# Kernel optimization log

Hardware: AMD Instinct MI355X
Metric: run time of the kernel (lower is better)

The kernel has to match this reference:

```python
import jax, jax.numpy as jnp
import numpy as np

I = 100000      # item_count
U = 131072      # user_count
E = 64          # embeddings_size
K = 3           # convolution_depth
TOPK = 15       # top_k nonzeros per row of S
NNZ_S = I * TOPK
NNZ_U = 4194304 # user-item interactions
KEEP = 0.8      # 1 - user_profile_dropout


def setup_inputs() -> dict:
    key = jax.random.key(0)
    k1, k2, k3, k4, k5, k6 = jax.random.split(key, 6)
    return {
        "item_emb": jax.random.normal(k1, (I, E), dtype=jnp.float32),
        "S_vals": jax.random.uniform(k2, (NNZ_S,), dtype=jnp.float32),
        "S_rows": jnp.sort(jax.random.randint(k3, (NNZ_S,), 0, I, dtype=jnp.int32)),
        "S_cols": jax.random.randint(k4, (NNZ_S,), 0, I, dtype=jnp.int32),
        "urm_vals": jnp.ones((NNZ_U,), dtype=jnp.float32),
        "urm_rows": jnp.sort(jax.random.randint(k5, (NNZ_U,), 0, U, dtype=jnp.int32)),
        "urm_cols": jax.random.randint(k6, (NNZ_U,), 0, I, dtype=jnp.int32),
    }


def _spmm(vals, rows, cols, x, n_rows):
    # sparse (COO) @ dense: gather source rows, scale by edge value, scatter-add.
    return jax.ops.segment_sum(vals[:, None] * x[cols], rows, num_segments=n_rows)


def reference(item_emb, S_vals, urm_vals, S_rows, S_cols, urm_rows, urm_cols):
    # sparse dropout on URM values (tf_dropout_sparse: drop + rescale by 1/keep)
    mask = jax.random.bernoulli(jax.random.key(42), KEEP, urm_vals.shape)
    uv = jnp.where(mask, urm_vals / KEEP, 0.0)
    # k-hop item-graph convolution: x <- S @ x, repeated K times
    x = item_emb
    for _ in range(K):
        x = _spmm(S_vals, S_rows, S_cols, x, I)
    # user embeddings: URM @ x
    user_emb = _spmm(uv, urm_rows, urm_cols, x, U)
    return user_emb, x
```

## Files before the change

### kernel.cpp

```cpp
#include <hip/hip_runtime.h>
#include <hip/hip_fp16.h>

#define I_CNT 100000
#define U_CNT 131072
#define E_DIM 64
#define IE (I_CNT * E_DIM)
#define UE ((size_t)U_CNT * E_DIM)

#define DEPTH 32

__device__ __forceinline__ unsigned rotl32(unsigned v, int n) {
    return (v << n) | (v >> (32 - n));
}
__device__ __forceinline__ void threefry2x32(unsigned k0, unsigned k1,
                                             unsigned x0, unsigned x1,
                                             unsigned& o0, unsigned& o1) {
    unsigned k2 = k0 ^ k1 ^ 0x1BD11BDAu;
    x0 += k0; x1 += k1;
#define RND(r) { x0 += x1; x1 = rotl32(x1, r); x1 ^= x0; }
    RND(13) RND(15) RND(26) RND(6)   x0 += k1; x1 += k2 + 1u;
    RND(17) RND(29) RND(16) RND(24)  x0 += k2; x1 += k0 + 2u;
    RND(13) RND(15) RND(26) RND(6)   x0 += k0; x1 += k1 + 3u;
    RND(17) RND(29) RND(16) RND(24)  x0 += k1; x1 += k2 + 4u;
    RND(13) RND(15) RND(26) RND(6)   x0 += k2; x1 += k0 + 5u;
#undef RND
    o0 = x0; o1 = x1;
}

__device__ __forceinline__ float dropout_mul(unsigned e) {
    unsigned o0, o1;
    threefry2x32(0u, 42u, 0u, e, o0, o1);
    const unsigned bits = o0 ^ o1;
    const float u = __uint_as_float((bits >> 9) | 0x3f800000u) - 1.0f;
    return (u < 0.8f) ? 1.25f : 0.0f;
}

__device__ __forceinline__ int rl_i(int v, int l) {
    return __builtin_amdgcn_readlane(v, l);
}
__device__ __forceinline__ float rl_f(float v, int l) {
    return __int_as_float(__builtin_amdgcn_readlane(__float_as_int(v), l));
}

__device__ __forceinline__ float2 unpack_h2(unsigned u) {
    float2 f;
    f.x = __half2float(__ushort_as_half((unsigned short)(u & 0xffffu)));
    f.y = __half2float(__ushort_as_half((unsigned short)(u >> 16)));
    return f;
}
__device__ __forceinline__ unsigned pack_h2(float a, float b) {
    const unsigned ha = __half_as_ushort(__float2half(a));
    const unsigned hb = __half_as_ushort(__float2half(b));
    return ha | (hb << 16);
}

__global__ void build_row_ptr(const int* __restrict__ rows,
                              int* __restrict__ row_ptr,
                              int nnz, int n_rows) {
    const int e = blockIdx.x * blockDim.x + threadIdx.x;
    if (e >= nnz) return;
    const int r  = rows[e];
    const int rp = (e == 0) ? -1 : rows[e - 1];
    for (int q = rp + 1; q <= r; ++q) row_ptr[q] = e;
    if (e == nnz - 1) {
        for (int q = r + 1; q <= n_rows; ++q) row_ptr[q] = nnz;
    }
}

__global__ __launch_bounds__(256) void f32_to_f16_vec(const float4* __restrict__ in,
                                                      unsigned long long* __restrict__ out,
                                                      int n4) {
    const int i = blockIdx.x * blockDim.x + threadIdx.x;
    if (i >= n4) return;
    const float4 f = in[i];
    const unsigned long long lo = pack_h2(f.x, f.y);
    const unsigned long long hi = pack_h2(f.z, f.w);
    __builtin_nontemporal_store(lo | (hi << 32), &out[i]);
}

template <bool DROPOUT, int NROWS, int SLOTS, bool OUT32, bool OUT16>
__global__ __launch_bounds__(256) void spmm_q(const float* __restrict__ vals,
                                              const int* __restrict__ row_ptr,
                                              const int* __restrict__ cols,
                                              const unsigned short* __restrict__ xh,
                                              float* __restrict__ y32,
                                              unsigned short* __restrict__ y16,
                                              int n_rows, int nnz) {
    constexpr int T     = NROWS * SLOTS;
    constexpr int QUADS = T / 4;
    constexpr int QPR   = SLOTS / 4;
    static_assert(T <= 64 && (SLOTS % 4) == 0, "slots must quad-align");

    const int lane = threadIdx.x & 63;
    const int wave = blockIdx.x * (blockDim.x >> 6) + (threadIdx.x >> 6);
    const int r0   = wave * NROWS;
    if (r0 >= n_rows) return;

    const int q  = min(lane / SLOTS, NROWS - 1);
    const int jr = lane - q * SLOTS;
    const int rq = r0 + q;

    const int s   = row_ptr[rq];
    const int e   = row_ptr[rq + 1];
    const int len = e - s;

    int ce = s + min(jr, max(len - 1, 0));
    ce = min(ce, nnz - 1);
    const int idx = __builtin_nontemporal_load(&cols[ce]);
    float v;
    {
        const int ve = min(s + jr, nnz - 1);
        float vv = __builtin_nontemporal_load(&vals[ve]);
        if (DROPOUT) vv *= dropout_mul((unsigned)ve);
        v = (jr < len) ? vv : 0.0f;
    }
    const int coff = idx << 7;

    const int g    = lane >> 4;
    const int m    = lane & 15;
    const int moff = m << 3;
    const char* __restrict__ xb = (const char*)xh;

    float4 ovf[NROWS];
#pragma unroll
    for (int qq = 0; qq < NROWS; ++qq) ovf[qq] = make_float4(0.f, 0.f, 0.f, 0.f);
    if (__any(len > SLOTS)) {
#pragma unroll
        for (int qq = 0; qq < NROWS; ++qq) {
            const int rs = rl_i(s, qq * SLOTS);
            const int re = rl_i(e, qq * SLOTS);
            for (int t = rs + SLOTS; t < re; ++t) {
                if (g == 0) {
                    const int c = cols[t];
                    float vv = vals[t];
                    if (DROPOUT) vv *= dropout_mul((unsigned)t);
                    const uint2 u = *(const uint2*)(xb + (c << 7) + moff);
                    const float2 f01 = unpack_h2(u.x);
                    const float2 f23 = unpack_h2(u.y);
                    ovf[qq].x = fmaf(vv, f01.x, ovf[qq].x);
                    ovf[qq].y = fmaf(vv, f01.y, ovf[qq].y);
                    ovf[qq].z = fmaf(vv, f23.x, ovf[qq].z);
                    ovf[qq].w = fmaf(vv, f23.y, ovf[qq].w);
                }
            }
        }
    }

    uint2 xq[QUADS];
#pragma unroll
    for (int k = 0; k < QUADS; ++k) {
        const int co = __shfl(coff, 4 * k + g);
        xq[k] = *(const uint2*)(xb + co + moff);
    }

    float4 acc = make_float4(0.f, 0.f, 0.f, 0.f);
#pragma unroll
    for (int k = 0; k < QUADS; ++k) {
        const float vv = __shfl(v, 4 * k + g);
        const float2 f01 = unpack_h2(xq[k].x);
        const float2 f23 = unpack_h2(xq[k].y);
        acc.x = fmaf(vv, f01.x, acc.x);
        acc.y = fmaf(vv, f01.y, acc.y);
        acc.z = fmaf(vv, f23.x, acc.z);
        acc.w = fmaf(vv, f23.y, acc.w);
        if ((k % QPR) == QPR - 1) {
            const int qk = k / QPR;
            float ax = acc.x + ovf[qk].x;
            float ay = acc.y + ovf[qk].y;
            float az = acc.z + ovf[qk].z;
            float aw = acc.w + ovf[qk].w;
            ax += __shfl_xor(ax, 16); ax += __shfl_xor(ax, 32);
            ay += __shfl_xor(ay, 16); ay += __shfl_xor(ay, 32);
            az += __shfl_xor(az, 16); az += __shfl_xor(az, 32);
            aw += __shfl_xor(aw, 16); aw += __shfl_xor(aw, 32);
            const size_t rowoff = ((size_t)(r0 + qk)) << 6;
            if (lane < 16) {
                if constexpr (OUT32) {
                    *(float4*)(y32 + rowoff + (m << 2)) = make_float4(ax, ay, az, aw);
                }
            } else if (lane < 32) {
                if constexpr (OUT16) {
                    const unsigned px = pack_h2(ax, ay);
                    const unsigned py = pack_h2(az, aw);
                    *(uint2*)(y16 + rowoff + (m << 2)) = make_uint2(px, py);
                }
            }
            acc = make_float4(0.f, 0.f, 0.f, 0.f);
        }
    }
    (void)y32; (void)y16;
}

template <bool DROPOUT, int NROWS, int SLOTS>
__global__ __launch_bounds__(256) void spmm_slots(const float* __restrict__ vals,
                                                  const int* __restrict__ row_ptr,
                                                  const int* __restrict__ cols,
                                                  const float* __restrict__ x,
                                                  float* __restrict__ y,
                                                  int n_rows, int nnz) {
    constexpr int T = NROWS * SLOTS;
    static_assert(T <= 64, "slots must fit one wave");
    constexpr int RING = (DEPTH < T) ? DEPTH : T;

    const int lane = threadIdx.x & 63;
    const int wave = blockIdx.x * (blockDim.x >> 6) + (threadIdx.x >> 6);
    const int r0   = wave * NROWS;
    if (r0 >= n_rows) return;

    const int q  = min(lane / SLOTS, NROWS - 1);
    const int j  = lane - q * SLOTS;
    const int rq = r0 + q;

    const int s   = row_ptr[rq];
    const int e   = row_ptr[rq + 1];
    const int len = e - s;

    int ce = s + min(j, max(len - 1, 0));
    ce = min(ce, nnz - 1);
    const int idx = cols[ce];
    float v;
    {
        const int ve = min(s + j, nnz - 1);
        float vv = vals[ve];
        if (DROPOUT) vv *= dropout_mul((unsigned)ve);
        v = (j < len) ? vv : 0.0f;
    }

    float ovf[NROWS];
#pragma unroll
    for (int qq = 0; qq < NROWS; ++qq) ovf[qq] = 0.0f;
    if (__any(len > SLOTS)) {
#pragma unroll
        for (int qq = 0; qq < NROWS; ++qq) {
            const int rs = rl_i(s, qq * SLOTS);
            const int re = rl_i(e, qq * SLOTS);
            for (int t = rs + SLOTS; t < re; ++t) {
                const int c = cols[t];
                float vv = vals[t];
                if (DROPOUT) vv *= dropout_mul((unsigned)t);
                ovf[qq] = fmaf(vv, x[((size_t)(unsigned)c << 6) + lane], ovf[qq]);
            }
        }
    }

    float xv[RING];
#pragma unroll
    for (int u = 0; u < RING; ++u) {
        xv[u] = x[((size_t)(unsigned)rl_i(idx, u) << 6) + lane];
    }

    float acc = 0.0f;
#pragma unroll
    for (int k = 0; k < T; ++k) {
        const float xc = xv[k % RING];
        if (k + RING < T) {
            xv[k % RING] = x[((size_t)(unsigned)rl_i(idx, k + RING) << 6) + lane];
        }
        acc = fmaf(rl_f(v, k), xc, acc);
        if ((k % SLOTS) == SLOTS - 1) {
            const int qk = k / SLOTS;
            y[((size_t)(r0 + qk) << 6) + lane] = acc + ovf[qk];
            acc = 0.0f;
        }
    }
}

static inline int blocks_for_waves(int waves) {
    return (waves + 3) / 4;
}

extern "C" void kernel_launch(void* const* d_in, const int* in_sizes, int n_in,
                              void* d_out, int out_size, void* d_ws, size_t ws_size,
                              hipStream_t stream) {
    const float* item_emb = (const float*)d_in[0];
    const float* S_vals   = (const float*)d_in[1];
    const int*   S_rows   = (const int*)  d_in[2];
    const int*   S_cols   = (const int*)  d_in[3];
    const float* urm_vals = (const float*)d_in[4];
    const int*   urm_rows = (const int*)  d_in[5];
    const int*   urm_cols = (const int*)  d_in[6];

    const int nnzS = in_sizes[1];
    const int nnzU = in_sizes[4];

    float* user_out = (float*)d_out;
    float* x_out    = (float*)d_out + UE;

    const size_t rpS_bytes = ((size_t)(I_CNT + 1) * sizeof(int) + 255) & ~(size_t)255;
    const size_t rpU_bytes = ((size_t)(U_CNT + 1) * sizeof(int) + 255) & ~(size_t)255;
    const size_t h_bytes   = (size_t)IE * sizeof(unsigned short);
    int* rpS = (int*)d_ws;
    int* rpU = (int*)((char*)d_ws + rpS_bytes);
    unsigned short* hA = (unsigned short*)((char*)d_ws + rpS_bytes + rpU_bytes);
    unsigned short* hB = (unsigned short*)((char*)hA + h_bytes);
    const size_t need = rpS_bytes + rpU_bytes + 2 * h_bytes;

    const dim3 blk(256);

    build_row_ptr<<<(nnzS + 255) / 256, blk, 0, stream>>>(S_rows, rpS, nnzS, I_CNT);
    build_row_ptr<<<(nnzU + 255) / 256, blk, 0, stream>>>(urm_rows, rpU, nnzU, U_CNT);

    const int wS = I_CNT / 2;

    if (ws_size >= need) {
        f32_to_f16_vec<<<(IE / 4 + 255) / 256, blk, 0, stream>>>(
            (const float4*)item_emb, (unsigned long long*)hA, IE / 4);

        spmm_q<false, 2, 24, false, true><<<blocks_for_waves(wS), blk, 0, stream>>>(
            S_vals, rpS, S_cols, hA, nullptr, hB, I_CNT, nnzS);
        spmm_q<false, 2, 24, false, true><<<blocks_for_waves(wS), blk, 0, stream>>>(
            S_vals, rpS, S_cols, hB, nullptr, hA, I_CNT, nnzS);
        spmm_q<false, 2, 24, true, true><<<blocks_for_waves(wS), blk, 0, stream>>>(
            S_vals, rpS, S_cols, hA, x_out, hB, I_CNT, nnzS);
        spmm_q<true, 1, 48, true, false><<<blocks_for_waves(U_CNT), blk, 0, stream>>>(
            urm_vals, rpU, urm_cols, hB, user_out, nullptr, U_CNT, nnzU);
    } else {
        spmm_slots<false, 2, 24><<<blocks_for_waves(wS), blk, 0, stream>>>(
            S_vals, rpS, S_cols, item_emb, x_out, I_CNT, nnzS);
        spmm_slots<false, 2, 24><<<blocks_for_waves(wS), blk, 0, stream>>>(
            S_vals, rpS, S_cols, x_out, user_out, I_CNT, nnzS);
        spmm_slots<false, 2, 24><<<blocks_for_waves(wS), blk, 0, stream>>>(
            S_vals, rpS, S_cols, user_out, x_out, I_CNT, nnzS);
        spmm_slots<true, 1, 48><<<blocks_for_waves(U_CNT), blk, 0, stream>>>(
            urm_vals, rpU, urm_cols, x_out, user_out, U_CNT, nnzU);
    }
}
```

Measured before the change: 303.8 us.

## Split embedding columns into four phases with blocked fp16 layout for cache reuse

The fp16 embedding buffers are rearranged into four column blocks of 16 features, each stored contiguously per row. Every SpMM now launches four phase-separated grids, each gathering only a 32-byte slice per row, so the gathered working set of each phase is small enough to stay cache-resident. The cost is that row pointers, columns and values are re-read once per phase, and each gathered row segment is now a narrower 32-byte access. A separate pre-pass also applies the URM dropout mask once up front, so the user SpMM no longer evaluates the random generator inline.

Measured after the change: 580.6 us. +91.1%, slower.

```diff
diff --git a/kernel.cpp b/kernel.cpp
--- a/kernel.cpp
+++ b/kernel.cpp
@@ -7,6 +7,7 @@
 #define IE (I_CNT * E_DIM)
 #define UE ((size_t)U_CNT * E_DIM)
 
+#define NPH 4
 #define DEPTH 32
 
 __device__ __forceinline__ unsigned rotl32(unsigned v, int n) {
@@ -67,59 +68,73 @@
     }
 }
 
-__global__ __launch_bounds__(256) void f32_to_f16_vec(const float4* __restrict__ in,
-                                                      unsigned long long* __restrict__ out,
+__global__ __launch_bounds__(256) void mask_vals(const float* __restrict__ vals,
+                                                 float* __restrict__ out, int nnz) {
+    const int e = blockIdx.x * blockDim.x + threadIdx.x;
+    if (e >= nnz) return;
+    __builtin_nontemporal_store(vals[e] * dropout_mul((unsigned)e), &out[e]);
+}
+
+__global__ __launch_bounds__(256) void f32_to_f16_blk(const float4* __restrict__ in,
+                                                      unsigned short* __restrict__ out,
                                                       int n4) {
     const int i = blockIdx.x * blockDim.x + threadIdx.x;
     if (i >= n4) return;
+    const int r   = i >> 4;
+    const int ii  = i & 15;
+    const int blk = ii >> 2;
+    const int mm  = ii & 3;
     const float4 f = in[i];
     const unsigned long long lo = pack_h2(f.x, f.y);
     const unsigned long long hi = pack_h2(f.z, f.w);
-    __builtin_nontemporal_store(lo | (hi << 32), &out[i]);
+    unsigned short* dst = out + ((size_t)blk * I_CNT + r) * 16 + (mm << 2);
+    __builtin_nontemporal_store(lo | (hi << 32), (unsigned long long*)dst);
 }
 
 template <bool DROPOUT, int NROWS, int SLOTS, bool OUT32, bool OUT16>
-__global__ __launch_bounds__(256) void spmm_q(const float* __restrict__ vals,
-                                              const int* __restrict__ row_ptr,
-                                              const int* __restrict__ cols,
-                                              const unsigned short* __restrict__ xh,
-                                              float* __restrict__ y32,
-                                              unsigned short* __restrict__ y16,
-                                              int n_rows, int nnz) {
-    constexpr int T     = NROWS * SLOTS;
-    constexpr int QUADS = T / 4;
-    constexpr int QPR   = SLOTS / 4;
-    static_assert(T <= 64 && (SLOTS % 4) == 0, "slots must quad-align");
-
-    const int lane = threadIdx.x & 63;
-    const int wave = blockIdx.x * (blockDim.x >> 6) + (threadIdx.x >> 6);
-    const int r0   = wave * NROWS;
+__global__ __launch_bounds__(256) void spmm_ph(const float* __restrict__ vals,
+                                               const int* __restrict__ row_ptr,
+                                               const int* __restrict__ cols,
+                                               const unsigned short* __restrict__ xh,
+                                               float* __restrict__ y32,
+                                               unsigned short* __restrict__ y16,
+                                               int n_rows, int nnz, int bpp) {
+    constexpr int T   = NROWS * SLOTS;
+    constexpr int LDN = T / 16;
+    constexpr int LPR = SLOTS / 16;
+    static_assert(T <= 64 && (SLOTS % 16) == 0, "slots must 16-align");
+
+    const int lane  = threadIdx.x & 63;
+    const int phase = blockIdx.x / bpp;
+    const int lblk  = blockIdx.x - phase * bpp;
+    const int wave  = lblk * (blockDim.x >> 6) + (threadIdx.x >> 6);
+    const int r0    = wave * NROWS;
     if (r0 >= n_rows) return;
 
     const int q  = min(lane / SLOTS, NROWS - 1);
-    const int jr = lane - q * SLOTS;
+    const int j  = lane - q * SLOTS;
     const int rq = r0 + q;
 
     const int s   = row_ptr[rq];
     const int e   = row_ptr[rq + 1];
     const int len = e - s;
 
-    int ce = s + min(jr, max(len - 1, 0));
+    int ce = s + min(j, max(len - 1, 0));
     ce = min(ce, nnz - 1);
     const int idx = __builtin_nontemporal_load(&cols[ce]);
     float v;
     {
-        const int ve = min(s + jr, nnz - 1);
+        const int ve = min(s + j, nnz - 1);
         float vv = __builtin_nontemporal_load(&vals[ve]);
         if (DROPOUT) vv *= dropout_mul((unsigned)ve);
-        v = (jr < len) ? vv : 0.0f;
-    }
-    const int coff = idx << 7;
-
-    const int g    = lane >> 4;
-    const int m    = lane & 15;
-    const int moff = m << 3;
-    const char* __restrict__ xb = (const char*)xh;
+        v = (j < len) ? vv : 0.0f;
+    }
+    const int coff = idx << 5;
+
+    const int g = lane >> 2;
+    const int m = lane & 3;
+    const char* __restrict__ xb =
+        (const char*)xh + (size_t)phase * ((size_t)I_CNT * 32);
 
     float4 ovf[NROWS];
 #pragma unroll
@@ -134,7 +149,7 @@
                     const int c = cols[t];
                     float vv = vals[t];
                     if (DROPOUT) vv *= dropout_mul((unsigned)t);
-                    const uint2 u = *(const uint2*)(xb + (c << 7) + moff);
+                    const uint2 u = *(const uint2*)(xb + (c << 5) + (m << 3));
                     const float2 f01 = unpack_h2(u.x);
                     const float2 f23 = unpack_h2(u.y);
                     ovf[qq].x = fmaf(vv, f01.x, ovf[qq].x);
@@ -146,43 +161,48 @@
         }
     }
 
-    uint2 xq[QUADS];
-#pragma unroll
-    for (int k = 0; k < QUADS; ++k) {
-        const int co = __shfl(coff, 4 * k + g);
-        xq[k] = *(const uint2*)(xb + co + moff);
+    uint2 xq[LDN];
+#pragma unroll
+    for (int k = 0; k < LDN; ++k) {
+        const int co = __shfl(coff, 16 * k + g);
+        xq[k] = *(const uint2*)(xb + co + (m << 3));
     }
 
     float4 acc = make_float4(0.f, 0.f, 0.f, 0.f);
 #pragma unroll
-    for (int k = 0; k < QUADS; ++k) {
-        const float vv = __shfl(v, 4 * k + g);
+    for (int k = 0; k < LDN; ++k) {
+        const float vv = __shfl(v, 16 * k + g);
         const float2 f01 = unpack_h2(xq[k].x);
         const float2 f23 = unpack_h2(xq[k].y);
         acc.x = fmaf(vv, f01.x, acc.x);
         acc.y = fmaf(vv, f01.y, acc.y);
         acc.z = fmaf(vv, f23.x, acc.z);
         acc.w = fmaf(vv, f23.y, acc.w);
-        if ((k % QPR) == QPR - 1) {
-            const int qk = k / QPR;
+        if ((k % LPR) == LPR - 1) {
+            const int qk = k / LPR;
             float ax = acc.x + ovf[qk].x;
             float ay = acc.y + ovf[qk].y;
             float az = acc.z + ovf[qk].z;
             float aw = acc.w + ovf[qk].w;
+            ax += __shfl_xor(ax, 4); ax += __shfl_xor(ax, 8);
             ax += __shfl_xor(ax, 16); ax += __shfl_xor(ax, 32);
+            ay += __shfl_xor(ay, 4); ay += __shfl_xor(ay, 8);
             ay += __shfl_xor(ay, 16); ay += __shfl_xor(ay, 32);
+            az += __shfl_xor(az, 4); az += __shfl_xor(az, 8);
             az += __shfl_xor(az, 16); az += __shfl_xor(az, 32);
+            aw += __shfl_xor(aw, 4); aw += __shfl_xor(aw, 8);
             aw += __shfl_xor(aw, 16); aw += __shfl_xor(aw, 32);
-            const size_t rowoff = ((size_t)(r0 + qk)) << 6;
-            if (lane < 16) {
+            const int row = r0 + qk;
+            if (lane < 4) {
                 if constexpr (OUT32) {
-                    *(float4*)(y32 + rowoff + (m << 2)) = make_float4(ax, ay, az, aw);
+                    *(float4*)(y32 + (size_t)row * E_DIM + phase * 16 + (m << 2)) =
+                        make_float4(ax, ay, az, aw);
                 }
-            } else if (lane < 32) {
                 if constexpr (OUT16) {
                     const unsigned px = pack_h2(ax, ay);
                     const unsigned py = pack_h2(az, aw);
-                    *(uint2*)(y16 + rowoff + (m << 2)) = make_uint2(px, py);
+                    *(uint2*)(y16 + ((size_t)phase * n_rows + row) * 16 + (m << 2)) =
+                        make_uint2(px, py);
                 }
             }
             acc = make_float4(0.f, 0.f, 0.f, 0.f);
@@ -286,35 +306,49 @@
     float* user_out = (float*)d_out;
     float* x_out    = (float*)d_out + UE;
 
-    const size_t rpS_bytes = ((size_t)(I_CNT + 1) * sizeof(int) + 255) & ~(size_t)255;
-    const size_t rpU_bytes = ((size_t)(U_CNT + 1) * sizeof(int) + 255) & ~(size_t)255;
-    const size_t h_bytes   = (size_t)IE * sizeof(unsigned short);
+    const size_t rpS_b = ((size_t)(I_CNT + 1) * 4 + 255) & ~(size_t)255;
+    const size_t rpU_b = ((size_t)(U_CNT + 1) * 4 + 255) & ~(size_t)255;
+    const size_t h_b   = (((size_t)IE * 2) + 255) & ~(size_t)255;
+    const size_t mv_b  = (((size_t)nnzU * 4) + 255) & ~(size_t)255;
     int* rpS = (int*)d_ws;
-    int* rpU = (int*)((char*)d_ws + rpS_bytes);
-    unsigned short* hA = (unsigned short*)((char*)d_ws + rpS_bytes + rpU_bytes);
-    unsigned short* hB = (unsigned short*)((char*)hA + h_bytes);
-    const size_t need = rpS_bytes + rpU_bytes + 2 * h_bytes;
+    int* rpU = (int*)((char*)d_ws + rpS_b);
+    unsigned short* hA = (unsigned short*)((char*)d_ws + rpS_b + rpU_b);
+    unsigned short* hB = (unsigned short*)((char*)hA + h_b);
+    float* mvU = (float*)((char*)hB + h_b);
+    const size_t need_base = rpS_b + rpU_b + 2 * h_b;
+    const size_t need_full = need_base + mv_b;
 
     const dim3 blk(256);
 
     build_row_ptr<<<(nnzS + 255) / 256, blk, 0, stream>>>(S_rows, rpS, nnzS, I_CNT);
     build_row_ptr<<<(nnzU + 255) / 256, blk, 0, stream>>>(urm_rows, rpU, nnzU, U_CNT);
 
-    const int wS = I_CNT / 2;
-
-    if (ws_size >= need) {
-        f32_to_f16_vec<<<(IE / 4 + 255) / 256, blk, 0, stream>>>(
-            (const float4*)item_emb, (unsigned long long*)hA, IE / 4);
-
-        spmm_q<false, 2, 24, false, true><<<blocks_for_waves(wS), blk, 0, stream>>>(
-            S_vals, rpS, S_cols, hA, nullptr, hB, I_CNT, nnzS);
-        spmm_q<false, 2, 24, false, true><<<blocks_for_waves(wS), blk, 0, stream>>>(
-            S_vals, rpS, S_cols, hB, nullptr, hA, I_CNT, nnzS);
-        spmm_q<false, 2, 24, true, true><<<blocks_for_waves(wS), blk, 0, stream>>>(
-            S_vals, rpS, S_cols, hA, x_out, hB, I_CNT, nnzS);
-        spmm_q<true, 1, 48, true, false><<<blocks_for_waves(U_CNT), blk, 0, stream>>>(
-            urm_vals, rpU, urm_cols, hB, user_out, nullptr, U_CNT, nnzU);
+    if (ws_size >= need_base) {
+        f32_to_f16_blk<<<(IE / 4 + 255) / 256, blk, 0, stream>>>(
+            (const float4*)item_emb, hA, IE / 4);
+
+        const int wS   = I_CNT / 2;
+        const int bppS = (blocks_for_waves(wS) + 0);
+        const dim3 gS(NPH * bppS);
+        spmm_ph<false, 2, 32, false, true><<<gS, blk, 0, stream>>>(
+            S_vals, rpS, S_cols, hA, nullptr, hB, I_CNT, nnzS, bppS);
+        spmm_ph<false, 2, 32, false, true><<<gS, blk, 0, stream>>>(
+            S_vals, rpS, S_cols, hB, nullptr, hA, I_CNT, nnzS, bppS);
+        spmm_ph<false, 2, 32, true, true><<<gS, blk, 0, stream>>>(
+            S_vals, rpS, S_cols, hA, x_out, hB, I_CNT, nnzS, bppS);
+
+        const int bppU = blocks_for_waves(U_CNT);
+        const dim3 gU(NPH * bppU);
+        if (ws_size >= need_full) {
+            mask_vals<<<(nnzU + 255) / 256, blk, 0, stream>>>(urm_vals, mvU, nnzU);
+            spmm_ph<false, 1, 48, true, false><<<gU, blk, 0, stream>>>(
+                mvU, rpU, urm_cols, hB, user_out, nullptr, U_CNT, nnzU, bppU);
+        } else {
+            spmm_ph<true, 1, 48, true, false><<<gU, blk, 0, stream>>>(
+                urm_vals, rpU, urm_cols, hB, user_out, nullptr, U_CNT, nnzU, bppU);
+        }
     } else {
+        const int wS = I_CNT / 2;
         spmm_slots<false, 2, 24><<<blocks_for_waves(wS), blk, 0, stream>>>(
             S_vals, rpS, S_cols, item_emb, x_out, I_CNT, nnzS);
         spmm_slots<false, 2, 24><<<blocks_for_waves(wS), blk, 0, stream>>>(
```
